# Kernel tuning notes

Measured on AMD Instinct MI355X. Metric: run time of the kernel, lower is better.

The kernel has to match this reference:

```python
import jax, jax.numpy as jnp
import numpy as np
import math

ALPHA = 0.1
LAMDA = 0.5
N_NODES = 100000
N_EDGES = 1600000
NLAYER = 4


def gcn_norm(edge_index, num_nodes):
    # symmetric GCN normalization with added self loops (fill value 1.0)
    loop = jnp.arange(num_nodes, dtype=edge_index.dtype)
    row = jnp.concatenate([edge_index[0], loop])
    col = jnp.concatenate([edge_index[1], loop])
    w = jnp.ones(row.shape[0], dtype=jnp.float32)
    deg = jax.ops.segment_sum(w, col, num_segments=num_nodes)
    dis = jnp.where(deg > 0, jax.lax.rsqrt(deg), 0.0)
    return row, col, dis[row] * w * dis[col]


def gcnii_conv(x, h0, w1, w2, beta, row, col, norm_w, num_nodes):
    # support/initial residual mixing (GCNII)
    support = (1.0 - beta) * (1.0 - ALPHA) * x + beta * (x @ w1)
    initial = (1.0 - beta) * ALPHA * h0 + beta * (h0 @ w2)
    # gather-scale-scatter: out[i] = sum_e norm_w[e] * support[row[e]] at col[e]
    msgs = norm_w[:, None] * support[row]
    agg = jax.ops.segment_sum(msgs, col, num_segments=num_nodes)
    return agg + initial


def setup_inputs() -> dict:
    key = jax.random.key(0)
    ks = jax.random.split(key, 8)
    # edges without self loops: col = (row + offset) % N, offset in [1, N-1]
    row = jax.random.randint(ks[0], (N_EDGES,), 0, N_NODES)
    off = jax.random.randint(ks[1], (N_EDGES,), 1, N_NODES)
    col = (row + off) % N_NODES
    edge_index = jnp.stack([row, col]).astype(jnp.int64)
    g = 0.1
    return {
        "x": jax.random.normal(ks[2], (N_NODES, 17), jnp.float32),
        "edge_index": edge_index,
        "W_in": jax.random.normal(ks[3], (17, 64), jnp.float32) * g,
        "b_in": jnp.zeros((64,), jnp.float32),
        "W1": jax.random.normal(ks[4], (NLAYER, 64, 64), jnp.float32) * g,
        "W2": jax.random.normal(ks[5], (NLAYER, 64, 64), jnp.float32) * g,
        "W_out": jax.random.normal(ks[6], (64, 2), jnp.float32) * g,
        "b_out": jnp.zeros((2,), jnp.float32),
    }


def reference(x, edge_index, W_in, b_in, W1, W2, W_out, b_out):
    num_nodes = x.shape[0]
    row, col, norm_w = gcn_norm(edge_index, num_nodes)
    # eval mode: dropout is identity
    h = jax.nn.relu(x @ W_in + b_in)
    h0 = h
    for i in range(NLAYER):
        beta = math.log(LAMDA / (i + 1) + 1.0)
        h = jax.nn.relu(gcnii_conv(h, h0, W1[i], W2[i], beta, row, col, norm_w, num_nodes))
    logits = h @ W_out + b_out
    return jax.nn.log_softmax(logits, axis=1)
```

## Files before the change

kernel.cpp:

```cpp
#include <hip/hip_runtime.h>
#include <math.h>

#define ALPHA_C 0.1f
#define EPB 4096

typedef __attribute__((ext_vector_type(4))) float f32x4;
typedef __attribute__((ext_vector_type(2))) float f32x2;
typedef __attribute__((ext_vector_type(8))) short bf16x8;

__device__ __forceinline__ float readlane_f(float v, int l) {
    return __int_as_float(__builtin_amdgcn_readlane(__float_as_int(v), l));
}

__device__ __forceinline__ unsigned short bf16_rtne(float f) {
    unsigned u = __float_as_uint(f);
    unsigned r = (u + 0x7FFFu + ((u >> 16) & 1u)) >> 16;
    return (unsigned short)r;
}

__device__ __forceinline__ float bflo(unsigned v) { return __uint_as_float(v << 16); }
__device__ __forceinline__ float bfhi(unsigned v) { return __uint_as_float(v & 0xFFFF0000u); }

__global__ void k_rhist(const int* __restrict__ col, int E, int span,
                        int* __restrict__ rangecount) {
    __shared__ int l[64];
    int tid = threadIdx.x;
    if (tid < 64) l[tid] = 0;
    __syncthreads();
    int base = blockIdx.x * EPB;
#pragma unroll
    for (int it = 0; it < 16; ++it) {
        int e = base + it * 256 + tid;
        if (e < E) atomicAdd(&l[(unsigned)col[e] / (unsigned)span], 1);
    }
    __syncthreads();
    if (tid < 64 && l[tid]) atomicAdd(&rangecount[tid], l[tid]);
}

__global__ void k_rscan(const int* __restrict__ rangecount,
                        int* __restrict__ rangeoffs, int E) {
    __shared__ int s[64];
    int tid = threadIdx.x;
    int v = rangecount[tid];
    s[tid] = v;
    __syncthreads();
    for (int d = 1; d < 64; d <<= 1) {
        int t = (tid >= d) ? s[tid - d] : 0;
        __syncthreads();
        s[tid] += t;
        __syncthreads();
    }
    rangeoffs[tid] = s[tid] - v;
    if (tid == 63) rangeoffs[64] = E;
}

__global__ void k_binA(const int* __restrict__ row, const int* __restrict__ col,
                       const int* __restrict__ rangeoffs, int* __restrict__ gcur,
                       uint2* __restrict__ staged, int E, int span) {
    __shared__ int lrun[64];
    int tid = threadIdx.x;
    int base = blockIdx.x * EPB;
    if (tid < 64) lrun[tid] = 0;
    __syncthreads();
#pragma unroll
    for (int it = 0; it < 16; ++it) {
        int e = base + it * 256 + tid;
        if (e < E) atomicAdd(&lrun[(unsigned)col[e] / (unsigned)span], 1);
    }
    __syncthreads();
    if (tid < 64) {
        int cnt = lrun[tid];
        int gb = cnt ? atomicAdd(&gcur[tid], cnt) : 0;
        lrun[tid] = rangeoffs[tid] + gb;
    }
    __syncthreads();
#pragma unroll
    for (int it = 0; it < 16; ++it) {
        int e = base + it * 256 + tid;
        if (e < E) {
            int c = col[e];
            int r = (unsigned)c / (unsigned)span;
            int pos = atomicAdd(&lrun[r], 1);
            staged[pos] = make_uint2((unsigned)c, (unsigned)row[e]);
        }
    }
}

__global__ void k_binB(const uint2* __restrict__ staged, const int* __restrict__ rangeoffs,
                       int* __restrict__ offs, float* __restrict__ dinv,
                       int* __restrict__ srcarr, int N, int span) {
    __shared__ int lcnt[1600];
    __shared__ int partial[256];
    int r = blockIdx.x;
    int tid = threadIdx.x;
    int nstart = r * span;
    if (nstart >= N) return;
    int nend = nstart + span; if (nend > N) nend = N;
    int cnt = nend - nstart;
    int estart = rangeoffs[r], eend = rangeoffs[r + 1];
    for (int t = tid; t < cnt; t += 256) lcnt[t] = 0;
    __syncthreads();
    for (int e = estart + tid; e < eend; e += 256)
        atomicAdd(&lcnt[(int)staged[e].x - nstart], 1);
    __syncthreads();
    int chunk = (cnt + 255) / 256;
    int c0 = tid * chunk; if (c0 > cnt) c0 = cnt;
    int c1 = c0 + chunk;  if (c1 > cnt) c1 = cnt;
    int sum = 0;
    for (int t = c0; t < c1; ++t) sum += lcnt[t];
    partial[tid] = sum;
    __syncthreads();
    for (int d = 1; d < 256; d <<= 1) {
        int t = (tid >= d) ? partial[tid - d] : 0;
        __syncthreads();
        partial[tid] += t;
        __syncthreads();
    }
    int run = estart + partial[tid] - sum;
    for (int t = c0; t < c1; ++t) {
        int c = lcnt[t];
        lcnt[t] = run;
        offs[nstart + t] = run;
        dinv[nstart + t] = rsqrtf(1.0f + (float)c);
        run += c;
    }
    if (nend == N && tid == 0) offs[N] = eend;
    __syncthreads();
    for (int e = estart + tid; e < eend; e += 256) {
        uint2 cr = staged[e];
        int idx = atomicAdd(&lcnt[(int)cr.x - nstart], 1);
        srcarr[idx] = (int)cr.y;
    }
}

__global__ void k_in(const float* __restrict__ x, const float* __restrict__ Win,
                     const float* __restrict__ bin, const float* __restrict__ dinv,
                     float* __restrict__ h0, unsigned short* __restrict__ g, int N) {
    int lane = threadIdx.x & 63;
    int wave = (blockIdx.x * blockDim.x + threadIdx.x) >> 6;
    int nwaves = (gridDim.x * blockDim.x) >> 6;
    float wreg[17];
#pragma unroll
    for (int k = 0; k < 17; ++k) wreg[k] = Win[k * 64 + lane];
    float breg = bin[lane];
    for (int i = wave; i < N; i += nwaves) {
        float xv = (lane < 17) ? x[i * 17 + lane] : 0.0f;
        float acc = breg;
#pragma unroll
        for (int k = 0; k < 17; ++k) acc += readlane_f(xv, k) * wreg[k];
        float r = fmaxf(acc, 0.0f);
        h0[(size_t)i * 64 + lane] = r;
        g[(size_t)i * 64 + lane] = bf16_rtne(dinv[i] * r);
    }
}

template <bool WRITE_G>
__global__ void k_gmix(const uint2* __restrict__ gp2, const float* __restrict__ h0,
                       const float* __restrict__ W1, const float* __restrict__ W2,
                       const float* __restrict__ dinv, const int* __restrict__ offs,
                       const int* __restrict__ srcarr, float beta,
                       float* __restrict__ of32, unsigned short* __restrict__ og16,
                       int N, int ntiles) {
    __shared__ float atile_s[4][16][68];
    int lane = threadIdx.x & 63;
    int wv = threadIdx.x >> 6;
    float (*atile)[68] = atile_s[wv];
    int r = lane & 15, q = lane >> 4;
    int wid = (blockIdx.x * blockDim.x + threadIdx.x) >> 6;
    int nw = (gridDim.x * blockDim.x) >> 6;
    float c1 = (1.0f - beta) * (1.0f - ALPHA_C);
    float c2 = (1.0f - beta) * ALPHA_C;

    bf16x8 bfrag[4][4];
#pragma unroll
    for (int c = 0; c < 4; ++c) {
#pragma unroll
        for (int ks = 0; ks < 4; ++ks) {
            int n = c * 16 + (lane & 15);
            int kb = ks * 32 + (lane >> 4) * 8;
            bf16x8 f;
#pragma unroll
            for (int j = 0; j < 8; ++j) {
                int k = kb + j;
                float w = (k < 64) ? beta * W1[k * 64 + n]
                                   : beta * W2[(k - 64) * 64 + n];
                f[j] = (short)bf16_rtne(w);
            }
            bfrag[c][ks] = f;
        }
    }

    for (int t = wid; t < ntiles; t += nw) {
        for (int ii = 0; ii < 16; ++ii) {
            int i = t * 16 + ii; if (i >= N) i = N - 1;
            int e0 = offs[i], e1 = offs[i + 1];
            float a0 = 0.0f, a1 = 0.0f, a2 = 0.0f, a3 = 0.0f;
            for (int base = e0; base < e1; base += 32) {
                int idx[8];
                uint2 v[8];
#pragma unroll
                for (int u = 0; u < 8; ++u) {
                    int eo = base + u * 4 + q;
                    idx[u] = srcarr[eo < e1 ? eo : e1 - 1];
                }
#pragma unroll
                for (int u = 0; u < 8; ++u) v[u] = gp2[(size_t)idx[u] * 16 + r];
#pragma unroll
                for (int u = 0; u < 8; ++u) {
                    bool ok = (base + u * 4 + q) < e1;
                    a0 += ok ? bflo(v[u].x) : 0.0f;
                    a1 += ok ? bfhi(v[u].x) : 0.0f;
                    a2 += ok ? bflo(v[u].y) : 0.0f;
                    a3 += ok ? bfhi(v[u].y) : 0.0f;
                }
            }
            a0 += __shfl_xor(a0, 16, 64); a0 += __shfl_xor(a0, 32, 64);
            a1 += __shfl_xor(a1, 16, 64); a1 += __shfl_xor(a1, 32, 64);
            a2 += __shfl_xor(a2, 16, 64); a2 += __shfl_xor(a2, 32, 64);
            a3 += __shfl_xor(a3, 16, 64); a3 += __shfl_xor(a3, 32, 64);
            if (q == 0) {
                uint2 sv = gp2[(size_t)i * 16 + r];
                float di = dinv[i];
                f32x4 w = {di * (a0 + bflo(sv.x)), di * (a1 + bfhi(sv.x)),
                           di * (a2 + bflo(sv.y)), di * (a3 + bfhi(sv.y))};
                *(f32x4*)&atile[ii][4 * r] = w;
                if (r == 0) atile[ii][66] = di;
            }
        }

        int rl = lane & 15;
        int koff = (lane >> 4) * 8;
        int grow = t * 16 + rl; if (grow >= N) grow = N - 1;
        f32x4 acc[4];
#pragma unroll
        for (int c = 0; c < 4; ++c) acc[c] = (f32x4){0.f, 0.f, 0.f, 0.f};
#pragma unroll
        for (int ks = 0; ks < 4; ++ks) {
            const float* sp = (ks < 2)
                ? &atile[rl][ks * 32 + koff]
                : &h0[(size_t)grow * 64 + (ks - 2) * 32 + koff];
            f32x4 lo = *(const f32x4*)sp;
            f32x4 hi = *(const f32x4*)(sp + 4);
            bf16x8 af;
#pragma unroll
            for (int j = 0; j < 4; ++j) af[j] = (short)bf16_rtne(lo[j]);
#pragma unroll
            for (int j = 0; j < 4; ++j) af[4 + j] = (short)bf16_rtne(hi[j]);
#pragma unroll
            for (int c = 0; c < 4; ++c)
                acc[c] = __builtin_amdgcn_mfma_f32_16x16x32_bf16(af, bfrag[c][ks], acc[c], 0, 0, 0);
        }

#pragma unroll
        for (int c = 0; c < 4; ++c) {
            int col = c * 16 + rl;
#pragma unroll
            for (int qq = 0; qq < 4; ++qq) {
                int row16 = (lane >> 4) * 4 + qq;
                int gr = t * 16 + row16;
                if (gr < N) {
                    size_t o = (size_t)gr * 64 + col;
                    float v = c1 * atile[row16][col] + c2 * h0[o] + acc[c][qq];
                    float rr = fmaxf(v, 0.0f);
                    if (WRITE_G) og16[o] = bf16_rtne(atile[row16][66] * rr);
                    else         of32[o] = rr;
                }
            }
        }
    }
}

__global__ void k_out(const float* __restrict__ h, const float* __restrict__ Wout,
                      const float* __restrict__ bout, float* __restrict__ out, int N) {
    int lane = threadIdx.x & 63;
    int wave = (blockIdx.x * blockDim.x + threadIdx.x) >> 6;
    int nwaves = (gridDim.x * blockDim.x) >> 6;
    float w0 = Wout[lane * 2 + 0], w1 = Wout[lane * 2 + 1];
    float b0 = bout[0], b1 = bout[1];
    for (int i = wave; i < N; i += nwaves) {
        float hv = h[(size_t)i * 64 + lane];
        float p0 = hv * w0, p1 = hv * w1;
#pragma unroll
        for (int d = 32; d > 0; d >>= 1) {
            p0 += __shfl_xor(p0, d, 64);
            p1 += __shfl_xor(p1, d, 64);
        }
        if (lane == 0) {
            float c0 = p0 + b0, c1 = p1 + b1;
            float m = fmaxf(c0, c1);
            float lse = m + logf(expf(c0 - m) + expf(c1 - m));
            out[(size_t)i * 2 + 0] = c0 - lse;
            out[(size_t)i * 2 + 1] = c1 - lse;
        }
    }
}

extern "C" void kernel_launch(void* const* d_in, const int* in_sizes, int n_in,
                              void* d_out, int out_size, void* d_ws, size_t ws_size,
                              hipStream_t stream) {
    const float* x    = (const float*)d_in[0];
    const int*   ei   = (const int*)d_in[1];
    const float* Win  = (const float*)d_in[2];
    const float* bin  = (const float*)d_in[3];
    const float* W1   = (const float*)d_in[4];
    const float* W2   = (const float*)d_in[5];
    const float* Wout = (const float*)d_in[6];
    const float* bout = (const float*)d_in[7];
    float* out = (float*)d_out;

    const int N = in_sizes[0] / 17;
    const int E = in_sizes[1] / 2;
    const int* rowp = ei;
    const int* colp = ei + E;
    const int span = (N + 63) / 64;

    char* p = (char*)d_ws;
    auto alloc = [&](size_t bytes) -> char* {
        char* r = p;
        p += (bytes + 255) & ~(size_t)255;
        return r;
    };
    int*   offs   = (int*)alloc((size_t)(N + 1) * sizeof(int));
    float* dinv   = (float*)alloc((size_t)N * sizeof(float));
    int*   rc_gc  = (int*)alloc(128 * sizeof(int));
    int*   roffs  = (int*)alloc(65 * sizeof(int));
    int*   srcarr = (int*)alloc((size_t)E * sizeof(int));
    size_t gbytes  = (size_t)N * 64 * sizeof(unsigned short);
    size_t stbytes = (size_t)E * sizeof(uint2);
    char*  stg    = alloc(stbytes > gbytes ? stbytes : gbytes);
    float*          h0   = (float*)alloc((size_t)N * 64 * sizeof(float));
    float*          hfin = (float*)alloc((size_t)N * 64 * sizeof(float));
    unsigned short* gA   = (unsigned short*)alloc(gbytes);
    uint2*          staged = (uint2*)stg;
    unsigned short* gB     = (unsigned short*)stg;

    int* rangecount = rc_gc;
    int* gcur       = rc_gc + 64;
    hipMemsetAsync(rc_gc, 0, 128 * sizeof(int), stream);

    const int TB = 256;
    const int nbA = (E + EPB - 1) / EPB;

    k_rhist<<<nbA, TB, 0, stream>>>(colp, E, span, rangecount);
    k_rscan<<<1, 64, 0, stream>>>(rangecount, roffs, E);
    k_binA<<<nbA, TB, 0, stream>>>(rowp, colp, roffs, gcur, staged, E, span);
    k_binB<<<64, TB, 0, stream>>>(staged, roffs, offs, dinv, srcarr, N, span);

    k_in<<<2048, TB, 0, stream>>>(x, Win, bin, dinv, h0, gA, N);

    const int ntiles = (N + 15) >> 4;

    for (int l = 0; l < 4; ++l) {
        float beta = logf(0.5f / (float)(l + 1) + 1.0f);
        const unsigned short* gin  = (l & 1) ? gB : gA;
        unsigned short*       gout = (l & 1) ? gA : gB;
        if (l < 3)
            k_gmix<true><<<1024, TB, 0, stream>>>((const uint2*)gin, h0,
                                                  W1 + (size_t)l * 4096, W2 + (size_t)l * 4096,
                                                  dinv, offs, srcarr, beta,
                                                  nullptr, gout, N, ntiles);
        else
            k_gmix<false><<<1024, TB, 0, stream>>>((const uint2*)gin, h0,
                                                   W1 + (size_t)l * 4096, W2 + (size_t)l * 4096,
                                                   dinv, offs, srcarr, beta,
                                                   hfin, nullptr, N, ntiles);
    }
    k_out<<<1024, TB, 0, stream>>>(hfin, Wout, bout, out, N);
}
```

Measured before the change: 462.3 us.

## Pack staging entries, prefold weights, store h0 in bf16, fuse output head

Result: faster. 445.5 us (-3.6%).

```diff
diff --git a/kernel.cpp b/kernel.cpp
--- a/kernel.cpp
+++ b/kernel.cpp
@@ -5,7 +5,6 @@
 #define EPB 4096
 
 typedef __attribute__((ext_vector_type(4))) float f32x4;
-typedef __attribute__((ext_vector_type(2))) float f32x2;
 typedef __attribute__((ext_vector_type(8))) short bf16x8;
 
 __device__ __forceinline__ float readlane_f(float v, int l) {
@@ -56,7 +55,7 @@
 
 __global__ void k_binA(const int* __restrict__ row, const int* __restrict__ col,
                        const int* __restrict__ rangeoffs, int* __restrict__ gcur,
-                       uint2* __restrict__ staged, int E, int span) {
+                       unsigned* __restrict__ staged, int E, int span) {
     __shared__ int lrun[64];
     int tid = threadIdx.x;
     int base = blockIdx.x * EPB;
@@ -81,12 +80,12 @@
             int c = col[e];
             int r = (unsigned)c / (unsigned)span;
             int pos = atomicAdd(&lrun[r], 1);
-            staged[pos] = make_uint2((unsigned)c, (unsigned)row[e]);
-        }
-    }
-}
-
-__global__ void k_binB(const uint2* __restrict__ staged, const int* __restrict__ rangeoffs,
+            staged[pos] = ((unsigned)row[e] << 11) | (unsigned)(c - r * span);
+        }
+    }
+}
+
+__global__ void k_binB(const unsigned* __restrict__ staged, const int* __restrict__ rangeoffs,
                        int* __restrict__ offs, float* __restrict__ dinv,
                        int* __restrict__ srcarr, int N, int span) {
     __shared__ int lcnt[1600];
@@ -101,7 +100,7 @@
     for (int t = tid; t < cnt; t += 256) lcnt[t] = 0;
     __syncthreads();
     for (int e = estart + tid; e < eend; e += 256)
-        atomicAdd(&lcnt[(int)staged[e].x - nstart], 1);
+        atomicAdd(&lcnt[staged[e] & 0x7FFu], 1);
     __syncthreads();
     int chunk = (cnt + 255) / 256;
     int c0 = tid * chunk; if (c0 > cnt) c0 = cnt;
@@ -127,15 +126,27 @@
     if (nend == N && tid == 0) offs[N] = eend;
     __syncthreads();
     for (int e = estart + tid; e < eend; e += 256) {
-        uint2 cr = staged[e];
-        int idx = atomicAdd(&lcnt[(int)cr.x - nstart], 1);
-        srcarr[idx] = (int)cr.y;
+        unsigned m = staged[e];
+        int idx = atomicAdd(&lcnt[m & 0x7FFu], 1);
+        srcarr[idx] = (int)(m >> 11);
+    }
+}
+
+__global__ void k_wfold(const float* __restrict__ W1, const float* __restrict__ W2,
+                        float beta, float c2, unsigned short* __restrict__ wf) {
+    int idx = blockIdx.x * 256 + threadIdx.x;
+    if (idx < 8192) {
+        int n = idx >> 7, k = idx & 127;
+        float w = (k < 64) ? beta * W1[k * 64 + n]
+                           : beta * W2[(k - 64) * 64 + n] + (((k - 64) == n) ? c2 : 0.0f);
+        wf[idx] = bf16_rtne(w);
     }
 }
 
 __global__ void k_in(const float* __restrict__ x, const float* __restrict__ Win,
                      const float* __restrict__ bin, const float* __restrict__ dinv,
-                     float* __restrict__ h0, unsigned short* __restrict__ g, int N) {
+                     unsigned short* __restrict__ h0b, unsigned short* __restrict__ g,
+                     int N) {
     int lane = threadIdx.x & 63;
     int wave = (blockIdx.x * blockDim.x + threadIdx.x) >> 6;
     int nwaves = (gridDim.x * blockDim.x) >> 6;
@@ -149,108 +160,98 @@
 #pragma unroll
         for (int k = 0; k < 17; ++k) acc += readlane_f(xv, k) * wreg[k];
         float r = fmaxf(acc, 0.0f);
-        h0[(size_t)i * 64 + lane] = r;
+        h0b[(size_t)i * 64 + lane] = bf16_rtne(r);
         g[(size_t)i * 64 + lane] = bf16_rtne(dinv[i] * r);
     }
 }
 
-template <bool WRITE_G>
-__global__ void k_gmix(const uint2* __restrict__ gp2, const float* __restrict__ h0,
-                       const float* __restrict__ W1, const float* __restrict__ W2,
+template <int MODE>
+__global__ void k_gmix(const uint2* __restrict__ gp2,
+                       const unsigned short* __restrict__ h0b,
+                       const unsigned short* __restrict__ wf,
                        const float* __restrict__ dinv, const int* __restrict__ offs,
-                       const int* __restrict__ srcarr, float beta,
-                       float* __restrict__ of32, unsigned short* __restrict__ og16,
+                       const int* __restrict__ srcarr, float c1,
+                       const float* __restrict__ Wout, const float* __restrict__ bout,
+                       float* __restrict__ out, unsigned short* __restrict__ og16,
                        int N, int ntiles) {
     __shared__ float atile_s[4][16][68];
     int lane = threadIdx.x & 63;
     int wv = threadIdx.x >> 6;
     float (*atile)[68] = atile_s[wv];
     int r = lane & 15, q = lane >> 4;
-    int wid = (blockIdx.x * blockDim.x + threadIdx.x) >> 6;
-    int nw = (gridDim.x * blockDim.x) >> 6;
-    float c1 = (1.0f - beta) * (1.0f - ALPHA_C);
-    float c2 = (1.0f - beta) * ALPHA_C;
-
+    int t = (blockIdx.x * blockDim.x + threadIdx.x) >> 6;
+    if (t >= ntiles) return;
+
+    int rl = lane & 15;
+    int koff = (lane >> 4) * 8;
     bf16x8 bfrag[4][4];
 #pragma unroll
-    for (int c = 0; c < 4; ++c) {
-#pragma unroll
-        for (int ks = 0; ks < 4; ++ks) {
-            int n = c * 16 + (lane & 15);
-            int kb = ks * 32 + (lane >> 4) * 8;
-            bf16x8 f;
-#pragma unroll
-            for (int j = 0; j < 8; ++j) {
-                int k = kb + j;
-                float w = (k < 64) ? beta * W1[k * 64 + n]
-                                   : beta * W2[(k - 64) * 64 + n];
-                f[j] = (short)bf16_rtne(w);
-            }
-            bfrag[c][ks] = f;
-        }
-    }
-
-    for (int t = wid; t < ntiles; t += nw) {
-        for (int ii = 0; ii < 16; ++ii) {
-            int i = t * 16 + ii; if (i >= N) i = N - 1;
-            int e0 = offs[i], e1 = offs[i + 1];
-            float a0 = 0.0f, a1 = 0.0f, a2 = 0.0f, a3 = 0.0f;
-            for (int base = e0; base < e1; base += 32) {
-                int idx[8];
-                uint2 v[8];
-#pragma unroll
-                for (int u = 0; u < 8; ++u) {
-                    int eo = base + u * 4 + q;
-                    idx[u] = srcarr[eo < e1 ? eo : e1 - 1];
-                }
-#pragma unroll
-                for (int u = 0; u < 8; ++u) v[u] = gp2[(size_t)idx[u] * 16 + r];
-#pragma unroll
-                for (int u = 0; u < 8; ++u) {
-                    bool ok = (base + u * 4 + q) < e1;
-                    a0 += ok ? bflo(v[u].x) : 0.0f;
-                    a1 += ok ? bfhi(v[u].x) : 0.0f;
-                    a2 += ok ? bflo(v[u].y) : 0.0f;
-                    a3 += ok ? bfhi(v[u].y) : 0.0f;
-                }
-            }
-            a0 += __shfl_xor(a0, 16, 64); a0 += __shfl_xor(a0, 32, 64);
-            a1 += __shfl_xor(a1, 16, 64); a1 += __shfl_xor(a1, 32, 64);
-            a2 += __shfl_xor(a2, 16, 64); a2 += __shfl_xor(a2, 32, 64);
-            a3 += __shfl_xor(a3, 16, 64); a3 += __shfl_xor(a3, 32, 64);
-            if (q == 0) {
-                uint2 sv = gp2[(size_t)i * 16 + r];
-                float di = dinv[i];
-                f32x4 w = {di * (a0 + bflo(sv.x)), di * (a1 + bfhi(sv.x)),
-                           di * (a2 + bflo(sv.y)), di * (a3 + bfhi(sv.y))};
-                *(f32x4*)&atile[ii][4 * r] = w;
-                if (r == 0) atile[ii][66] = di;
-            }
-        }
-
-        int rl = lane & 15;
-        int koff = (lane >> 4) * 8;
-        int grow = t * 16 + rl; if (grow >= N) grow = N - 1;
-        f32x4 acc[4];
-#pragma unroll
-        for (int c = 0; c < 4; ++c) acc[c] = (f32x4){0.f, 0.f, 0.f, 0.f};
-#pragma unroll
-        for (int ks = 0; ks < 4; ++ks) {
-            const float* sp = (ks < 2)
-                ? &atile[rl][ks * 32 + koff]
-                : &h0[(size_t)grow * 64 + (ks - 2) * 32 + koff];
+    for (int c = 0; c < 4; ++c)
+#pragma unroll
+        for (int ks = 0; ks < 4; ++ks)
+            bfrag[c][ks] = *(const bf16x8*)&wf[(c * 16 + rl) * 128 + ks * 32 + koff];
+
+    for (int ii = 0; ii < 16; ++ii) {
+        int i = t * 16 + ii; if (i >= N) i = N - 1;
+        int e0 = offs[i], e1 = offs[i + 1];
+        float a0 = 0.0f, a1 = 0.0f, a2 = 0.0f, a3 = 0.0f;
+        for (int base = e0; base < e1; base += 32) {
+            int idx[8];
+            uint2 v[8];
+#pragma unroll
+            for (int u = 0; u < 8; ++u) {
+                int eo = base + u * 4 + q;
+                idx[u] = srcarr[eo < e1 ? eo : e1 - 1];
+            }
+#pragma unroll
+            for (int u = 0; u < 8; ++u) v[u] = gp2[(size_t)idx[u] * 16 + r];
+#pragma unroll
+            for (int u = 0; u < 8; ++u) {
+                bool ok = (base + u * 4 + q) < e1;
+                a0 += ok ? bflo(v[u].x) : 0.0f;
+                a1 += ok ? bfhi(v[u].x) : 0.0f;
+                a2 += ok ? bflo(v[u].y) : 0.0f;
+                a3 += ok ? bfhi(v[u].y) : 0.0f;
+            }
+        }
+        a0 += __shfl_xor(a0, 16, 64); a0 += __shfl_xor(a0, 32, 64);
+        a1 += __shfl_xor(a1, 16, 64); a1 += __shfl_xor(a1, 32, 64);
+        a2 += __shfl_xor(a2, 16, 64); a2 += __shfl_xor(a2, 32, 64);
+        a3 += __shfl_xor(a3, 16, 64); a3 += __shfl_xor(a3, 32, 64);
+        if (q == 0) {
+            uint2 sv = gp2[(size_t)i * 16 + r];
+            float di = dinv[i];
+            f32x4 w = {di * (a0 + bflo(sv.x)), di * (a1 + bfhi(sv.x)),
+                       di * (a2 + bflo(sv.y)), di * (a3 + bfhi(sv.y))};
+            *(f32x4*)&atile[ii][4 * r] = w;
+            if (r == 0) atile[ii][66] = di;
+        }
+    }
+
+    int grow = t * 16 + rl; if (grow >= N) grow = N - 1;
+    f32x4 acc[4];
+#pragma unroll
+    for (int c = 0; c < 4; ++c) acc[c] = (f32x4){0.f, 0.f, 0.f, 0.f};
+#pragma unroll
+    for (int ks = 0; ks < 4; ++ks) {
+        bf16x8 af;
+        if (ks < 2) {
+            const float* sp = &atile[rl][ks * 32 + koff];
             f32x4 lo = *(const f32x4*)sp;
             f32x4 hi = *(const f32x4*)(sp + 4);
-            bf16x8 af;
 #pragma unroll
             for (int j = 0; j < 4; ++j) af[j] = (short)bf16_rtne(lo[j]);
 #pragma unroll
             for (int j = 0; j < 4; ++j) af[4 + j] = (short)bf16_rtne(hi[j]);
-#pragma unroll
-            for (int c = 0; c < 4; ++c)
-                acc[c] = __builtin_amdgcn_mfma_f32_16x16x32_bf16(af, bfrag[c][ks], acc[c], 0, 0, 0);
-        }
-
+        } else {
+            af = *(const bf16x8*)&h0b[(size_t)grow * 64 + (ks - 2) * 32 + koff];
+        }
+#pragma unroll
+        for (int c = 0; c < 4; ++c)
+            acc[c] = __builtin_amdgcn_mfma_f32_16x16x32_bf16(af, bfrag[c][ks], acc[c], 0, 0, 0);
+    }
+
+    if (MODE == 0) {
 #pragma unroll
         for (int c = 0; c < 4; ++c) {
             int col = c * 16 + rl;
@@ -259,38 +260,51 @@
                 int row16 = (lane >> 4) * 4 + qq;
                 int gr = t * 16 + row16;
                 if (gr < N) {
-                    size_t o = (size_t)gr * 64 + col;
-                    float v = c1 * atile[row16][col] + c2 * h0[o] + acc[c][qq];
+                    float v = c1 * atile[row16][col] + acc[c][qq];
                     float rr = fmaxf(v, 0.0f);
-                    if (WRITE_G) og16[o] = bf16_rtne(atile[row16][66] * rr);
-                    else         of32[o] = rr;
+                    og16[(size_t)gr * 64 + col] = bf16_rtne(atile[row16][66] * rr);
                 }
             }
         }
-    }
-}
-
-__global__ void k_out(const float* __restrict__ h, const float* __restrict__ Wout,
-                      const float* __restrict__ bout, float* __restrict__ out, int N) {
-    int lane = threadIdx.x & 63;
-    int wave = (blockIdx.x * blockDim.x + threadIdx.x) >> 6;
-    int nwaves = (gridDim.x * blockDim.x) >> 6;
-    float w0 = Wout[lane * 2 + 0], w1 = Wout[lane * 2 + 1];
-    float b0 = bout[0], b1 = bout[1];
-    for (int i = wave; i < N; i += nwaves) {
-        float hv = h[(size_t)i * 64 + lane];
-        float p0 = hv * w0, p1 = hv * w1;
-#pragma unroll
-        for (int d = 32; d > 0; d >>= 1) {
-            p0 += __shfl_xor(p0, d, 64);
-            p1 += __shfl_xor(p1, d, 64);
-        }
-        if (lane == 0) {
-            float c0 = p0 + b0, c1 = p1 + b1;
-            float m = fmaxf(c0, c1);
-            float lse = m + logf(expf(c0 - m) + expf(c1 - m));
-            out[(size_t)i * 2 + 0] = c0 - lse;
-            out[(size_t)i * 2 + 1] = c1 - lse;
+    } else {
+        float w0c[4], w1c[4];
+#pragma unroll
+        for (int c = 0; c < 4; ++c) {
+            int col = c * 16 + rl;
+            w0c[c] = Wout[col * 2 + 0];
+            w1c[c] = Wout[col * 2 + 1];
+        }
+        float b0 = bout[0], b1 = bout[1];
+        float hq[4][4];
+#pragma unroll
+        for (int c = 0; c < 4; ++c) {
+            int col = c * 16 + rl;
+#pragma unroll
+            for (int qq = 0; qq < 4; ++qq) {
+                int row16 = (lane >> 4) * 4 + qq;
+                hq[c][qq] = fmaxf(c1 * atile[row16][col] + acc[c][qq], 0.0f);
+            }
+        }
+#pragma unroll
+        for (int qq = 0; qq < 4; ++qq) {
+            float p0 = hq[0][qq] * w0c[0] + hq[1][qq] * w0c[1]
+                     + hq[2][qq] * w0c[2] + hq[3][qq] * w0c[3];
+            float p1 = hq[0][qq] * w1c[0] + hq[1][qq] * w1c[1]
+                     + hq[2][qq] * w1c[2] + hq[3][qq] * w1c[3];
+#pragma unroll
+            for (int d = 1; d < 16; d <<= 1) {
+                p0 += __shfl_xor(p0, d, 64);
+                p1 += __shfl_xor(p1, d, 64);
+            }
+            int row16 = (lane >> 4) * 4 + qq;
+            int gr = t * 16 + row16;
+            if (rl == 0 && gr < N) {
+                float l0 = p0 + b0, l1 = p1 + b1;
+                float m = fmaxf(l0, l1);
+                float lse = m + logf(expf(l0 - m) + expf(l1 - m));
+                out[(size_t)gr * 2 + 0] = l0 - lse;
+                out[(size_t)gr * 2 + 1] = l1 - lse;
+            }
         }
     }
 }
@@ -320,18 +334,18 @@
         p += (bytes + 255) & ~(size_t)255;
         return r;
     };
-    int*   offs   = (int*)alloc((size_t)(N + 1) * sizeof(int));
-    float* dinv   = (float*)alloc((size_t)N * sizeof(float));
-    int*   rc_gc  = (int*)alloc(128 * sizeof(int));
-    int*   roffs  = (int*)alloc(65 * sizeof(int));
-    int*   srcarr = (int*)alloc((size_t)E * sizeof(int));
+    int*      offs   = (int*)alloc((size_t)(N + 1) * sizeof(int));
+    float*    dinv   = (float*)alloc((size_t)N * sizeof(float));
+    int*      rc_gc  = (int*)alloc(128 * sizeof(int));
+    int*      roffs  = (int*)alloc(65 * sizeof(int));
+    int*      srcarr = (int*)alloc((size_t)E * sizeof(int));
+    unsigned short* wfold = (unsigned short*)alloc(4 * 8192 * sizeof(unsigned short));
     size_t gbytes  = (size_t)N * 64 * sizeof(unsigned short);
-    size_t stbytes = (size_t)E * sizeof(uint2);
+    size_t stbytes = (size_t)E * sizeof(unsigned);
     char*  stg    = alloc(stbytes > gbytes ? stbytes : gbytes);
-    float*          h0   = (float*)alloc((size_t)N * 64 * sizeof(float));
-    float*          hfin = (float*)alloc((size_t)N * 64 * sizeof(float));
-    unsigned short* gA   = (unsigned short*)alloc(gbytes);
-    uint2*          staged = (uint2*)stg;
+    unsigned short* h0b = (unsigned short*)alloc(gbytes);
+    unsigned short* gA  = (unsigned short*)alloc(gbytes);
+    unsigned*       staged = (unsigned*)stg;
     unsigned short* gB     = (unsigned short*)stg;
 
     int* rangecount = rc_gc;
@@ -346,24 +360,33 @@
     k_binA<<<nbA, TB, 0, stream>>>(rowp, colp, roffs, gcur, staged, E, span);
     k_binB<<<64, TB, 0, stream>>>(staged, roffs, offs, dinv, srcarr, N, span);
 
-    k_in<<<2048, TB, 0, stream>>>(x, Win, bin, dinv, h0, gA, N);
-
-    const int ntiles = (N + 15) >> 4;
-
+    k_in<<<2048, TB, 0, stream>>>(x, Win, bin, dinv, h0b, gA, N);
     for (int l = 0; l < 4; ++l) {
         float beta = logf(0.5f / (float)(l + 1) + 1.0f);
+        float c2 = (1.0f - beta) * ALPHA_C;
+        k_wfold<<<32, TB, 0, stream>>>(W1 + (size_t)l * 4096, W2 + (size_t)l * 4096,
+                                       beta, c2, wfold + (size_t)l * 8192);
+    }
+
+    const int ntiles = (N + 15) >> 4;
+    const int nbG = (ntiles + 3) / 4;
+
+    for (int l = 0; l < 4; ++l) {
+        float beta = logf(0.5f / (float)(l + 1) + 1.0f);
+        float c1 = (1.0f - beta) * (1.0f - ALPHA_C);
         const unsigned short* gin  = (l & 1) ? gB : gA;
         unsigned short*       gout = (l & 1) ? gA : gB;
         if (l < 3)
-            k_gmix<true><<<1024, TB, 0, stream>>>((const uint2*)gin, h0,
-                                                  W1 + (size_t)l * 4096, W2 + (size_t)l * 4096,
-                                                  dinv, offs, srcarr, beta,
-                                                  nullptr, gout, N, ntiles);
+            k_gmix<0><<<nbG, TB, 0, stream>>>((const uint2*)gin, h0b,
+                                              wfold + (size_t)l * 8192,
+                                              dinv, offs, srcarr, c1,
+                                              nullptr, nullptr, nullptr, gout,
+                                              N, ntiles);
         else
-            k_gmix<false><<<1024, TB, 0, stream>>>((const uint2*)gin, h0,
-                                                   W1 + (size_t)l * 4096, W2 + (size_t)l * 4096,
-                                                   dinv, offs, srcarr, beta,
-                                                   hfin, nullptr, N, ntiles);
-    }
-    k_out<<<1024, TB, 0, stream>>>(hfin, Wout, bout, out, N);
-}
+            k_gmix<1><<<nbG, TB, 0, stream>>>((const uint2*)gin, h0b,
+                                              wfold + (size_t)l * 8192,
+                                              dinv, offs, srcarr, c1,
+                                              Wout, bout, out, nullptr,
+                                              N, ntiles);
+    }
+}
```
